# Kernel optimization log

Hardware: AMD Instinct MI355X
Metric: run time of the kernel (lower is better)

Reference implementation:

```python
import jax, jax.numpy as jnp
import numpy as np

N_EXPERTS = 64
TOP_K = 8
NORM_TOPK = True
SCALING = 1.0


def setup_inputs() -> dict:
    key = jax.random.key(0)
    logits = jax.random.normal(key, (524288, N_EXPERTS), dtype=jnp.float32)
    return {"logits": logits}


def reference(logits):
    # scoring_func == 'softmax': softmax over expert dim in float32
    routing_weights = jax.nn.softmax(logits.astype(jnp.float32), axis=1)
    # top-k experts per token: values and indices, sorted descending (matches torch.topk)
    topk_weights, topk_ids = jax.lax.top_k(routing_weights, TOP_K)  # [T, K]
    if NORM_TOPK:
        topk_weights = topk_weights / jnp.sum(topk_weights, axis=-1, keepdims=True)
    if SCALING != 1.0:
        topk_weights = topk_weights * SCALING
    # torch.histc(topk_ids, bins=E, min=0, max=E) == bincount over flat ids (float output)
    tokens_per_expert = jnp.zeros((N_EXPERTS,), dtype=jnp.float32).at[topk_ids.ravel()].add(1.0)
    return (logits, routing_weights, topk_weights, topk_ids, tokens_per_expert)
```

## Files before the change

kernel.cpp:

```cpp
#include <hip/hip_runtime.h>
#include <math.h>

#define NEXP 64
#define TOPK 8
#define SB 512
#define PITCH 65
#define GRID 256

typedef float v4 __attribute__((ext_vector_type(4)));

__global__ __launch_bounds__(SB, 2) void router_kernel(
    const float* __restrict__ logits,
    float* __restrict__ out_logits,
    float* __restrict__ out_rw,
    float* __restrict__ out_tw,
    float* __restrict__ out_ti,
    float* __restrict__ out_hist,
    int nSB)
{
    __shared__ float tile[SB * PITCH];
    __shared__ float srow[SB];
    __shared__ float shist[NEXP];

    const int tid = threadIdx.x;
    if (tid < NEXP) shist[tid] = 0.0f;

    const int stride = gridDim.x;
    int s = blockIdx.x;

    v4 pre[16];
    {
        const v4* g = (const v4*)logits + (long)s * SB * (NEXP / 4);
        #pragma unroll
        for (int k = 0; k < 16; ++k)
            pre[k] = __builtin_nontemporal_load(&g[tid + (k << 9)]);
    }

    for (; s < nSB; s += stride) {
        const long tokBase = (long)s * SB;
        const long vbase   = tokBase * (NEXP / 4);

        v4* gpass = (v4*)out_logits + vbase;
        #pragma unroll
        for (int k = 0; k < 16; ++k) {
            int i = tid + (k << 9);
            v4 v = pre[k];
            gpass[i] = v;
            int r  = i >> 4;
            int c4 = (i & 15) << 2;
            float* b = &tile[r * PITCH + c4];
            b[0] = v.x; b[1] = v.y; b[2] = v.z; b[3] = v.w;
        }
        __syncthreads();

        const int ns = s + stride;
        if (ns < nSB) {
            const v4* g = (const v4*)logits + (long)ns * SB * (NEXP / 4);
            #pragma unroll
            for (int k = 0; k < 16; ++k)
                pre[k] = __builtin_nontemporal_load(&g[tid + (k << 9)]);
        }

        float* __restrict__ row = &tile[tid * PITCH];
        float vals[TOPK], ids[TOPK];
        #pragma unroll
        for (int j = 0; j < TOPK; ++j) { vals[j] = -INFINITY; ids[j] = 0.0f; }
        float ssum = 0.0f;

        #pragma unroll 8
        for (int e = 0; e < NEXP; ++e) {
            float x  = row[e];
            float ev = __expf(x);
            ssum += ev;
            row[e] = ev;
            float fe = (float)e;
            bool c[TOPK];
            #pragma unroll
            for (int j = 0; j < TOPK; ++j) c[j] = x > vals[j];
            #pragma unroll
            for (int j = TOPK - 1; j >= 1; --j) {
                ids[j]  = c[j] ? (c[j - 1] ? ids[j - 1] : fe) : ids[j];
                vals[j] = __builtin_amdgcn_fmed3f(x, vals[j - 1], vals[j]);
            }
            ids[0]  = c[0] ? fe : ids[0];
            vals[0] = fmaxf(vals[0], x);
        }
        const float sinv = 1.0f / ssum;
        srow[tid] = sinv;

        float ew[TOPK];
        float tsum = 0.0f;
        #pragma unroll
        for (int j = 0; j < TOPK; ++j) { ew[j] = __expf(vals[j]); tsum += ew[j]; }
        const float tinv = 1.0f / tsum;

        const long tok = tokBase + tid;
        v4* twp = (v4*)out_tw + tok * 2;
        v4* tip = (v4*)out_ti + tok * 2;
        v4 w0 = { ew[0] * tinv, ew[1] * tinv, ew[2] * tinv, ew[3] * tinv };
        v4 w1 = { ew[4] * tinv, ew[5] * tinv, ew[6] * tinv, ew[7] * tinv };
        v4 i0 = { ids[0], ids[1], ids[2], ids[3] };
        v4 i1 = { ids[4], ids[5], ids[6], ids[7] };
        twp[0] = w0; twp[1] = w1;
        tip[0] = i0; tip[1] = i1;

        #pragma unroll
        for (int j = 0; j < TOPK; ++j)
            atomicAdd(&shist[(int)ids[j]], 1.0f);

        __syncthreads();

        v4* grw = (v4*)out_rw + vbase;
        #pragma unroll
        for (int k = 0; k < 16; ++k) {
            int i  = tid + (k << 9);
            int r  = i >> 4;
            int c4 = (i & 15) << 2;
            float si = srow[r];
            const float* b = &tile[r * PITCH + c4];
            v4 o = { b[0] * si, b[1] * si, b[2] * si, b[3] * si };
            grw[i] = o;
        }
        __syncthreads();
    }

    if (tid < NEXP) atomicAdd(&out_hist[tid], shist[tid]);
}

extern "C" void kernel_launch(void* const* d_in, const int* in_sizes, int n_in,
                              void* d_out, int out_size, void* d_ws, size_t ws_size,
                              hipStream_t stream) {
    const float* logits = (const float*)d_in[0];
    const long T = (long)in_sizes[0] / NEXP;

    float* out      = (float*)d_out;
    float* o_logits = out;
    float* o_rw     = out + T * NEXP;
    float* o_tw     = out + 2 * T * NEXP;
    float* o_ti     = o_tw + T * TOPK;
    float* o_hist   = o_ti + T * TOPK;

    (void)hipMemsetAsync(o_hist, 0, NEXP * sizeof(float), stream);

    const int nSB  = (int)(T / SB);
    const int grid = nSB < GRID ? nSB : GRID;
    router_kernel<<<grid, SB, 0, stream>>>(logits, o_logits, o_rw, o_tw, o_ti,
                                           o_hist, nSB);
}
```

Measured before the change: 102.9 us.

## Warp-specialize producer and consumer waves with double-buffered LDS tiles

Splits each 512-thread block into 4 producer waves and 4 consumer waves. Producers load the next 256-token tile, write the logits passthrough, stage the tile into a double-buffered LDS slot, and write the previous tile's normalized softmax. Consumers run exp/top-k on the current tile. This overlaps global memory traffic with compute and cuts barriers per iteration from three to one. In exchange, only half the threads do compute per tile, occupancy hints change (launch_bounds min-blocks removed), and LDS use per block stays about the same.

```diff
diff --git a/kernel.cpp b/kernel.cpp
--- a/kernel.cpp
+++ b/kernel.cpp
@@ -3,127 +3,159 @@
 
 #define NEXP 64
 #define TOPK 8
-#define SB 512
+#define TTILE 256
 #define PITCH 65
+#define NPROD 4
+#define BLKT 512
 #define GRID 256
 
 typedef float v4 __attribute__((ext_vector_type(4)));
 
-__global__ __launch_bounds__(SB, 2) void router_kernel(
+__global__ __launch_bounds__(BLKT) void router_kernel(
     const float* __restrict__ logits,
     float* __restrict__ out_logits,
     float* __restrict__ out_rw,
     float* __restrict__ out_tw,
     float* __restrict__ out_ti,
     float* __restrict__ out_hist,
-    int nSB)
+    int nT)
 {
-    __shared__ float tile[SB * PITCH];
-    __shared__ float srow[SB];
+    __shared__ float lds[2][TTILE * PITCH];
+    __shared__ float srow[2][TTILE];
     __shared__ float shist[NEXP];
 
-    const int tid = threadIdx.x;
+    const int tid  = threadIdx.x;
+    const int wid  = tid >> 6;
+    const int l    = tid & 63;
+    const bool prod = wid < NPROD;
     if (tid < NEXP) shist[tid] = 0.0f;
 
-    const int stride = gridDim.x;
-    int s = blockIdx.x;
+    const int G = gridDim.x;
+    int tb = blockIdx.x;
+    v4 regs[16];
 
-    v4 pre[16];
-    {
-        const v4* g = (const v4*)logits + (long)s * SB * (NEXP / 4);
+    if (prod && tb < nT) {
+        const long base = (long)tb * (TTILE * NEXP / 4);
+        const v4* g = (const v4*)logits + base;
         #pragma unroll
         for (int k = 0; k < 16; ++k)
-            pre[k] = __builtin_nontemporal_load(&g[tid + (k << 9)]);
-    }
-
-    for (; s < nSB; s += stride) {
-        const long tokBase = (long)s * SB;
-        const long vbase   = tokBase * (NEXP / 4);
-
-        v4* gpass = (v4*)out_logits + vbase;
+            regs[k] = __builtin_nontemporal_load(&g[(wid << 6) + l + (k << 8)]);
+        v4* gp = (v4*)out_logits + base;
         #pragma unroll
         for (int k = 0; k < 16; ++k) {
-            int i = tid + (k << 9);
-            v4 v = pre[k];
-            gpass[i] = v;
-            int r  = i >> 4;
-            int c4 = (i & 15) << 2;
-            float* b = &tile[r * PITCH + c4];
+            int i = (wid << 6) + l + (k << 8);
+            v4 v = regs[k];
+            gp[i] = v;
+            int r = i >> 4, c4 = (i & 15) << 2;
+            float* b = &lds[0][r * PITCH + c4];
             b[0] = v.x; b[1] = v.y; b[2] = v.z; b[3] = v.w;
         }
-        __syncthreads();
+    }
+    __syncthreads();
 
-        const int ns = s + stride;
-        if (ns < nSB) {
-            const v4* g = (const v4*)logits + (long)ns * SB * (NEXP / 4);
+    int it = 0;
+    for (; tb < nT; ++it, tb += G) {
+        const int cur = it & 1;
+        const int nxt = cur ^ 1;
+        const int tb_next = tb + G;
+
+        if (prod) {
+            if (tb_next < nT) {
+                const v4* g = (const v4*)logits + (long)tb_next * (TTILE * NEXP / 4);
+                #pragma unroll
+                for (int k = 0; k < 16; ++k)
+                    regs[k] = __builtin_nontemporal_load(&g[(wid << 6) + l + (k << 8)]);
+            }
+            if (it > 0) {
+                v4* grw = (v4*)out_rw + (long)(tb - G) * (TTILE * NEXP / 4);
+                #pragma unroll
+                for (int k = 0; k < 16; ++k) {
+                    int i = (wid << 6) + l + (k << 8);
+                    int r = i >> 4, c4 = (i & 15) << 2;
+                    float si = srow[nxt][r];
+                    const float* b = &lds[nxt][r * PITCH + c4];
+                    v4 o = { b[0] * si, b[1] * si, b[2] * si, b[3] * si };
+                    grw[i] = o;
+                }
+            }
+            if (tb_next < nT) {
+                v4* gp = (v4*)out_logits + (long)tb_next * (TTILE * NEXP / 4);
+                #pragma unroll
+                for (int k = 0; k < 16; ++k) {
+                    int i = (wid << 6) + l + (k << 8);
+                    v4 v = regs[k];
+                    gp[i] = v;
+                    int r = i >> 4, c4 = (i & 15) << 2;
+                    float* b = &lds[nxt][r * PITCH + c4];
+                    b[0] = v.x; b[1] = v.y; b[2] = v.z; b[3] = v.w;
+                }
+            }
+        } else {
+            const int t = ((wid - NPROD) << 6) + l;
+            float* __restrict__ row = &lds[cur][t * PITCH];
+            float vals[TOPK], ids[TOPK];
             #pragma unroll
-            for (int k = 0; k < 16; ++k)
-                pre[k] = __builtin_nontemporal_load(&g[tid + (k << 9)]);
-        }
+            for (int j = 0; j < TOPK; ++j) { vals[j] = -INFINITY; ids[j] = 0.0f; }
+            float ssum = 0.0f;
 
-        float* __restrict__ row = &tile[tid * PITCH];
-        float vals[TOPK], ids[TOPK];
-        #pragma unroll
-        for (int j = 0; j < TOPK; ++j) { vals[j] = -INFINITY; ids[j] = 0.0f; }
-        float ssum = 0.0f;
+            #pragma unroll 8
+            for (int e = 0; e < NEXP; ++e) {
+                float x  = row[e];
+                float ev = __expf(x);
+                ssum += ev;
+                row[e] = ev;
+                float fe = (float)e;
+                bool c[TOPK];
+                #pragma unroll
+                for (int j = 0; j < TOPK; ++j) c[j] = x > vals[j];
+                #pragma unroll
+                for (int j = TOPK - 1; j >= 1; --j) {
+                    ids[j]  = c[j] ? (c[j - 1] ? ids[j - 1] : fe) : ids[j];
+                    vals[j] = __builtin_amdgcn_fmed3f(x, vals[j - 1], vals[j]);
+                }
+                ids[0]  = c[0] ? fe : ids[0];
+                vals[0] = fmaxf(vals[0], x);
+            }
+            const float sinv = 1.0f / ssum;
+            srow[cur][t] = sinv;
 
-        #pragma unroll 8
-        for (int e = 0; e < NEXP; ++e) {
-            float x  = row[e];
-            float ev = __expf(x);
-            ssum += ev;
-            row[e] = ev;
-            float fe = (float)e;
-            bool c[TOPK];
+            float ew[TOPK];
+            float tsum = 0.0f;
             #pragma unroll
-            for (int j = 0; j < TOPK; ++j) c[j] = x > vals[j];
+            for (int j = 0; j < TOPK; ++j) { ew[j] = __expf(vals[j]); tsum += ew[j]; }
+            const float tinv = 1.0f / tsum;
+
+            const long tok = (long)tb * TTILE + t;
+            v4* twp = (v4*)out_tw + tok * 2;
+            v4* tip = (v4*)out_ti + tok * 2;
+            v4 w0 = { ew[0] * tinv, ew[1] * tinv, ew[2] * tinv, ew[3] * tinv };
+            v4 w1 = { ew[4] * tinv, ew[5] * tinv, ew[6] * tinv, ew[7] * tinv };
+            v4 i0 = { ids[0], ids[1], ids[2], ids[3] };
+            v4 i1 = { ids[4], ids[5], ids[6], ids[7] };
+            twp[0] = w0; twp[1] = w1;
+            tip[0] = i0; tip[1] = i1;
+
             #pragma unroll
-            for (int j = TOPK - 1; j >= 1; --j) {
-                ids[j]  = c[j] ? (c[j - 1] ? ids[j - 1] : fe) : ids[j];
-                vals[j] = __builtin_amdgcn_fmed3f(x, vals[j - 1], vals[j]);
-            }
-            ids[0]  = c[0] ? fe : ids[0];
-            vals[0] = fmaxf(vals[0], x);
-        }
-        const float sinv = 1.0f / ssum;
-        srow[tid] = sinv;
-
-        float ew[TOPK];
-        float tsum = 0.0f;
-        #pragma unroll
-        for (int j = 0; j < TOPK; ++j) { ew[j] = __expf(vals[j]); tsum += ew[j]; }
-        const float tinv = 1.0f / tsum;
-
-        const long tok = tokBase + tid;
-        v4* twp = (v4*)out_tw + tok * 2;
-        v4* tip = (v4*)out_ti + tok * 2;
-        v4 w0 = { ew[0] * tinv, ew[1] * tinv, ew[2] * tinv, ew[3] * tinv };
-        v4 w1 = { ew[4] * tinv, ew[5] * tinv, ew[6] * tinv, ew[7] * tinv };
-        v4 i0 = { ids[0], ids[1], ids[2], ids[3] };
-        v4 i1 = { ids[4], ids[5], ids[6], ids[7] };
-        twp[0] = w0; twp[1] = w1;
-        tip[0] = i0; tip[1] = i1;
-
-        #pragma unroll
-        for (int j = 0; j < TOPK; ++j)
-            atomicAdd(&shist[(int)ids[j]], 1.0f);
-
-        __syncthreads();
-
-        v4* grw = (v4*)out_rw + vbase;
-        #pragma unroll
-        for (int k = 0; k < 16; ++k) {
-            int i  = tid + (k << 9);
-            int r  = i >> 4;
-            int c4 = (i & 15) << 2;
-            float si = srow[r];
-            const float* b = &tile[r * PITCH + c4];
-            v4 o = { b[0] * si, b[1] * si, b[2] * si, b[3] * si };
-            grw[i] = o;
+            for (int j = 0; j < TOPK; ++j)
+                atomicAdd(&shist[(int)ids[j]], 1.0f);
         }
         __syncthreads();
     }
 
+    if (prod && it > 0) {
+        const int lastpar = (it - 1) & 1;
+        v4* grw = (v4*)out_rw + (long)(tb - G) * (TTILE * NEXP / 4);
+        #pragma unroll
+        for (int k = 0; k < 16; ++k) {
+            int i = (wid << 6) + l + (k << 8);
+            int r = i >> 4, c4 = (i & 15) << 2;
+            float si = srow[lastpar][r];
+            const float* b = &lds[lastpar][r * PITCH + c4];
+            v4 o = { b[0] * si, b[1] * si, b[2] * si, b[3] * si };
+            grw[i] = o;
+        }
+    }
+    __syncthreads();
     if (tid < NEXP) atomicAdd(&out_hist[tid], shist[tid]);
 }
 
@@ -142,8 +174,8 @@
 
     (void)hipMemsetAsync(o_hist, 0, NEXP * sizeof(float), stream);
 
-    const int nSB  = (int)(T / SB);
-    const int grid = nSB < GRID ? nSB : GRID;
-    router_kernel<<<grid, SB, 0, stream>>>(logits, o_logits, o_rw, o_tw, o_ti,
-                                           o_hist, nSB);
+    const int nT   = (int)(T / TTILE);
+    const int grid = nT < GRID ? nT : GRID;
+    router_kernel<<<grid, BLKT, 0, stream>>>(logits, o_logits, o_rw, o_tw, o_ti,
+                                             o_hist, nT);
 }
```

After: 88.71 us (median of 2 runs). 1.16x faster.
